# Optimization experiments

Hardware: AMD Instinct MI355X
Metric: run time of the kernel (lower is better)

## Reference

```python
import jax, jax.numpy as jnp
import numpy as np

N, E, C, ED = 50000, 800000, 128, 16
NEG_SLOPE = 0.2


def setup_inputs() -> dict:
    key = jax.random.key(0)
    ks = jax.random.split(key, 18)
    inp = {
        "h": jax.random.normal(ks[0], (N, C), jnp.float32),
        "edge_index": jax.random.randint(ks[1], (2, E), 0, N),
        "edge_attr": jax.random.normal(ks[2], (E, ED), jnp.float32),
        "reducible": jax.random.randint(ks[3], (N,), 0, 2) > 0,
    }
    names = ["W", "att_src", "att_dst", "W_edge", "att_edge", "W_res", "bias"]
    shapes = [(C, C), (C,), (C,), (ED, C), (C,), (C, C), (C,)]
    i = 4
    for pre in ["red_", "irr_"]:
        for n, sh in zip(names, shapes):
            inp[pre + n] = jax.random.normal(ks[i], sh, jnp.float32) * 0.05
            i += 1
    return inp


def _gat_conv(h, src, dst, edge_attr, W, att_src, att_dst, W_edge, att_edge, W_res, bias):
    """PyG GATConv (heads=1, residual=True, add_self_loops=True, fill_value='mean')."""
    n = h.shape[0]
    # self-loop edge_attr = mean of incoming edge_attr per node (0 if none)
    sum_attr = jax.ops.segment_sum(edge_attr, dst, num_segments=n)
    cnt = jax.ops.segment_sum(jnp.ones((edge_attr.shape[0],), edge_attr.dtype), dst, num_segments=n)
    mean_attr = sum_attr / jnp.maximum(cnt, 1.0)[:, None]
    loop = jnp.arange(n)
    s = jnp.concatenate([src, loop])   # [E+N]
    d = jnp.concatenate([dst, loop])   # [E+N]
    ea = jnp.concatenate([edge_attr, mean_attr], axis=0)  # [E+N, ED]
    x = h @ W                              # [N, C]
    a_src = x @ att_src                    # [N]
    a_dst = x @ att_dst                    # [N]
    a_edge = (ea @ W_edge) @ att_edge      # [E+N]
    alpha = jax.nn.leaky_relu(a_src[s] + a_dst[d] + a_edge, NEG_SLOPE)
    # per-destination softmax (every node has a self-loop -> denom > 0)
    m = jax.ops.segment_max(alpha, d, num_segments=n)
    ex = jnp.exp(alpha - m[d])
    denom = jax.ops.segment_sum(ex, d, num_segments=n)
    w = ex / denom[d]                      # [E+N]
    out = jax.ops.segment_sum(w[:, None] * x[s], d, num_segments=n)  # [N, C]
    return out + h @ W_res + bias


def reference(h, edge_index, edge_attr, reducible,
              red_W, red_att_src, red_att_dst, red_W_edge, red_att_edge, red_W_res, red_bias,
              irr_W, irr_att_src, irr_att_dst, irr_W_edge, irr_att_edge, irr_W_res, irr_bias):
    src, dst = edge_index[0], edge_index[1]
    out_r = _gat_conv(h, src, dst, edge_attr, red_W, red_att_src, red_att_dst,
                      red_W_edge, red_att_edge, red_W_res, red_bias)
    out_i = _gat_conv(h, src, dst, edge_attr, irr_W, irr_att_src, irr_att_dst,
                      irr_W_edge, irr_att_edge, irr_W_res, irr_bias)
    return jax.nn.relu(jnp.where(reducible[:, None], out_r, out_i))
```

## Files before the change

kernel.cpp:

```cpp
#include <hip/hip_runtime.h>
#include <hip/hip_bf16.h>

#define CDIM 128
#define EDIM 16
#define NEG_SLOPE 0.2f

typedef __attribute__((ext_vector_type(8))) short bf16x8;
typedef __attribute__((ext_vector_type(4))) float f32x4;
typedef __attribute__((ext_vector_type(2))) float f32x2;
typedef unsigned int uint;
typedef unsigned short ushort;

__device__ __forceinline__ ushort f2bf(float f) {
    uint u = __float_as_uint(f);
    return (ushort)((u + 0x7fffu + ((u >> 16) & 1u)) >> 16);
}
__device__ __forceinline__ uint packbf(float lo, float hi) {
    return ((uint)f2bf(hi) << 16) | (uint)f2bf(lo);
}
__device__ __forceinline__ float bflo(uint w) { return __uint_as_float(w << 16); }
__device__ __forceinline__ float bfhi(uint w) { return __uint_as_float(w & 0xffff0000u); }

__device__ __forceinline__ bool redtest(const void* red, int i, int notInt, int notFloat) {
    if (!notInt)        return ((const int*)red)[i] != 0;
    else if (!notFloat) return ((const float*)red)[i] != 0.f;
    else                return ((const unsigned char*)red)[i] != 0;
}

__global__ void bcatwe_kernel(const float* __restrict__ Wr, const float* __restrict__ Wi,
                              const float* __restrict__ Wrr, const float* __restrict__ Wri,
                              ushort* __restrict__ BT,
                              const float* __restrict__ WeR, const float* __restrict__ aeR,
                              const float* __restrict__ WeI, const float* __restrict__ aeI,
                              float* __restrict__ we) {
    if (blockIdx.x < 256) {
        int idx = blockIdx.x * 256 + threadIdx.x;
        int c = idx >> 7, k = idx & 127;
        const float* srcm;
        if (c < 128)      srcm = Wr;
        else if (c < 256) srcm = Wi;
        else if (c < 384) srcm = Wrr;
        else              srcm = Wri;
        BT[idx] = f2bf(srcm[k * 128 + (c & 127)]);
    } else {
        int lane = threadIdx.x;
        if (lane < 16) {
            float s = 0.f;
            for (int c = 0; c < CDIM; ++c) s += WeR[lane * CDIM + c] * aeR[c];
            we[lane] = s;
        } else if (lane < 32) {
            int j = lane - 16;
            float s = 0.f;
            for (int c = 0; c < CDIM; ++c) s += WeI[j * CDIM + c] * aeI[c];
            we[16 + j] = s;
        }
    }
}

__global__ __launch_bounds__(256) void prep_kernel(const uint* __restrict__ red, int nwords,
                                                   int* __restrict__ flags,
                                                   const int* __restrict__ dst, int* __restrict__ cnt8,
                                                   int* __restrict__ rank,
                                                   const float* __restrict__ ea, const float* __restrict__ we,
                                                   uint* __restrict__ escal4,
                                                   const float* __restrict__ h, ushort* __restrict__ hbf,
                                                   int N, int E, int n4) {
    int i = blockIdx.x * 256 + threadIdx.x;
    int c = blockIdx.x & 7;
    if (i < nwords) {
        uint w = red[i];
        bool isInt = (w <= 1u);
        bool isFloat = (w == 0u) || (w == 0x3f800000u);
        if (!isInt) atomicOr(&flags[0], 1);
        if (!isFloat) atomicOr(&flags[1], 1);
    }
    if (i < E) {
        int d = dst[i];
        int rk = atomicAdd(&cnt8[c * N + d], 1);
        __builtin_nontemporal_store(rk | (c << 28), rank + i);
        const f32x4* row = (const f32x4*)(ea + (size_t)i * EDIM);
        const float4* we4 = (const float4*)we;
        float er = 0.f, ei = 0.f;
#pragma unroll
        for (int q = 0; q < 4; ++q) {
            f32x4 v = __builtin_nontemporal_load(row + q);
            float4 wr = we4[q], wi = we4[4 + q];
            er += v.x * wr.x + v.y * wr.y + v.z * wr.z + v.w * wr.w;
            ei += v.x * wi.x + v.y * wi.y + v.z * wi.z + v.w * wi.w;
        }
        __builtin_nontemporal_store(packbf(er, ei), escal4 + i);
    }
    if (i < n4) {
        f32x4 v = __builtin_nontemporal_load((const f32x4*)h + i);
        uint2 o;
        o.x = packbf(v.x, v.y);
        o.y = packbf(v.z, v.w);
        ((uint2*)hbf)[i] = o;
    }
}

__global__ __launch_bounds__(256) void gemm_dots(const ushort* __restrict__ A,
                                                 const ushort* __restrict__ BT,
                                                 ushort* __restrict__ C,
                                                 const float* __restrict__ attsr, const float* __restrict__ attdr,
                                                 const float* __restrict__ attsi, const float* __restrict__ attdi,
                                                 float* __restrict__ asr, float* __restrict__ adr,
                                                 float* __restrict__ asi, float* __restrict__ adi,
                                                 int M) {
    __shared__ ushort As[128 * 128];
    __shared__ ushort Bs[128 * 128];
    __shared__ float dots[4][128];
    int t = threadIdx.x;
    int lane = t & 63, wv = t >> 6;
    int rb = blockIdx.x * 128;

    if (t < 128) { dots[0][t] = 0.f; dots[1][t] = 0.f; dots[2][t] = 0.f; dots[3][t] = 0.f; }

    int rsub = wv * 4 + (lane >> 4);
    int c0 = lane & 15;
#pragma unroll
    for (int p = 0; p < 8; ++p) {
        int row = p * 16 + rsub;
        int chunk = c0 ^ (row & 7);
        int gra = rb + row; if (gra > M - 1) gra = M - 1;
        const ushort* ga = A + (size_t)gra * 128 + chunk * 8;
        __builtin_amdgcn_global_load_lds(
            (const __attribute__((address_space(1))) void*)ga,
            (__attribute__((address_space(3))) void*)((char*)As + p * 4096 + wv * 1024),
            16, 0, 0);
    }

    int wr = wv >> 1, wc = wv & 1;
    int l15 = lane & 15, l4 = lane >> 4;
    const char* Ab = (const char*)As;
    const char* Bb = (const char*)Bs;

    for (int s = 0; s < 4; ++s) {
#pragma unroll
        for (int p = 0; p < 8; ++p) {
            int row = p * 16 + rsub;
            int chunk = c0 ^ (row & 7);
            const ushort* gb = BT + (size_t)(s * 128 + row) * 128 + chunk * 8;
            __builtin_amdgcn_global_load_lds(
                (const __attribute__((address_space(1))) void*)gb,
                (__attribute__((address_space(3))) void*)((char*)Bs + p * 4096 + wv * 1024),
                16, 0, 0);
        }
        __syncthreads();

        f32x4 acc[4][4];
#pragma unroll
        for (int i = 0; i < 4; ++i)
#pragma unroll
            for (int j = 0; j < 4; ++j) acc[i][j] = (f32x4){0.f, 0.f, 0.f, 0.f};

#pragma unroll
        for (int ks = 0; ks < 4; ++ks) {
            bf16x8 a[4], b[4];
#pragma unroll
            for (int f = 0; f < 4; ++f) {
                int row = wr * 64 + f * 16 + l15;
                int ch = (ks * 4 + l4) ^ (row & 7);
                a[f] = *(const bf16x8*)(Ab + row * 256 + ch * 16);
                int col = wc * 64 + f * 16 + l15;
                int ch2 = (ks * 4 + l4) ^ (col & 7);
                b[f] = *(const bf16x8*)(Bb + col * 256 + ch2 * 16);
            }
#pragma unroll
            for (int i = 0; i < 4; ++i)
#pragma unroll
                for (int j = 0; j < 4; ++j)
                    acc[i][j] = __builtin_amdgcn_mfma_f32_16x16x32_bf16(a[i], b[j], acc[i][j], 0, 0, 0);
        }

        if (s < 2) {
            const float* attS = s ? attsi : attsr;
            const float* attD = s ? attdi : attdr;
            float aS[4], aD[4];
#pragma unroll
            for (int j = 0; j < 4; ++j) {
                int c = wc * 64 + j * 16 + l15;
                aS[j] = attS[c]; aD[j] = attD[c];
            }
#pragma unroll
            for (int i = 0; i < 4; ++i)
#pragma unroll
                for (int rr = 0; rr < 4; ++rr) {
                    float ps = 0.f, pd = 0.f;
#pragma unroll
                    for (int j = 0; j < 4; ++j) {
                        float v = acc[i][j][rr];
                        ps += v * aS[j]; pd += v * aD[j];
                    }
#pragma unroll
                    for (int d = 1; d < 16; d <<= 1) {
                        ps += __shfl_xor(ps, d); pd += __shfl_xor(pd, d);
                    }
                    if (l15 == 0) {
                        int row = wr * 64 + i * 16 + l4 * 4 + rr;
                        atomicAdd(&dots[s * 2 + 0][row], ps);
                        atomicAdd(&dots[s * 2 + 1][row], pd);
                    }
                }
        }

#pragma unroll
        for (int i = 0; i < 4; ++i) {
            int rl = wr * 64 + i * 16 + l4 * 4;
#pragma unroll
            for (int j = 0; j < 4; ++j) {
                int col = s * 128 + wc * 64 + j * 16 + l15;
#pragma unroll
                for (int r = 0; r < 4; ++r) {
                    int gr = rb + rl + r;
                    if (gr < M) C[(size_t)gr * 512 + col] = f2bf(acc[i][j][r]);
                }
            }
        }
        __syncthreads();
    }

    if (t < 128) {
        int gr = rb + t;
        if (gr < M) {
            asr[gr] = dots[0][t]; adr[gr] = dots[1][t];
            asi[gr] = dots[2][t]; adi[gr] = dots[3][t];
        }
    }
}

__global__ __launch_bounds__(256) void scanA_kernel(int* __restrict__ cnt8,
                                                    int* __restrict__ offA,
                                                    int* __restrict__ bsum, int n) {
    __shared__ int wsum[4];
    int t = threadIdx.x, lane = t & 63, wid = t >> 6;
    int i0 = blockIdx.x * 1024 + t * 4;
    int v[4];
#pragma unroll
    for (int j = 0; j < 4; ++j) {
        int d = i0 + j;
        int tot = 0;
        if (d < n) {
#pragma unroll
            for (int x = 0; x < 8; ++x) {
                int cv = cnt8[x * n + d];
                cnt8[x * n + d] = tot;
                tot += cv;
            }
        }
        v[j] = tot;
    }
    int s = v[0] + v[1] + v[2] + v[3];
    int incl = s;
#pragma unroll
    for (int d = 1; d < 64; d <<= 1) { int u = __shfl_up(incl, d); if (lane >= d) incl += u; }
    if (lane == 63) wsum[wid] = incl;
    __syncthreads();
    int wpre = 0;
    for (int w = 0; w < wid; ++w) wpre += wsum[w];
    int run = wpre + incl - s;
#pragma unroll
    for (int j = 0; j < 4; ++j) {
        int i = i0 + j;
        if (i < n) offA[i] = run;
        run += v[j];
    }
    if (t == 255) bsum[blockIdx.x] = wpre + incl;
}

__global__ void scanB_kernel(int* __restrict__ bsum, int nb) {
    int lane = threadIdx.x;
    int carry = 0;
    for (int base = 0; base < nb; base += 64) {
        int i = base + lane;
        int v = (i < nb) ? bsum[i] : 0;
        int incl = v;
#pragma unroll
        for (int d = 1; d < 64; d <<= 1) { int u = __shfl_up(incl, d); if (lane >= d) incl += u; }
        if (i < nb) bsum[i] = carry + incl - v;
        carry += __shfl(incl, 63);
    }
}

__global__ __launch_bounds__(256) void scatter_kernel(
    const int* __restrict__ src, const int* __restrict__ dst,
    const int* __restrict__ rank, const uint* __restrict__ escal4,
    const void* __restrict__ red, const int* __restrict__ flags,
    const int* __restrict__ offA, const int* __restrict__ bsum,
    const int* __restrict__ cnt8,
    uint* __restrict__ csr, int N, int E) {
    int e = blockIdx.x * 256 + threadIdx.x;
    if (e >= E) return;
    int s = __builtin_nontemporal_load(src + e);
    int d = __builtin_nontemporal_load(dst + e);
    uint ee = __builtin_nontemporal_load(escal4 + e);
    int rkw = __builtin_nontemporal_load(rank + e);
    int c = ((uint)rkw) >> 28;
    int rk = rkw & 0x0fffffff;
    int notInt = flags[0], notFloat = flags[1];
    bool rr = redtest(red, d, notInt, notFloat);
    uint evb = rr ? (ee & 0xffffu) : (ee >> 16);
    int off = offA[d] + bsum[d >> 10] + cnt8[c * N + d];
    csr[off + rk] = (uint)s | (evb << 16);
}

__global__ __launch_bounds__(256) void node_kernel(
    const ushort* __restrict__ xcat,
    const float* __restrict__ adst_r, const float* __restrict__ adst_i,
    const float* __restrict__ asrc_r, const float* __restrict__ asrc_i,
    const void* __restrict__ red, const int* __restrict__ flags,
    const int* __restrict__ offA, const int* __restrict__ bsum,
    const uint* __restrict__ csr,
    const float* __restrict__ bias_r, const float* __restrict__ bias_i,
    float* __restrict__ out, int n, int E) {
    __shared__ uint2 buf[4][64];
    int wv = threadIdx.x >> 6, lane = threadIdx.x & 63;
    int node = blockIdx.x * 4 + wv;
    if (node >= n) return;

    int notInt = flags[0], notFloat = flags[1];
    bool r = redtest(red, node, notInt, notFloat);

    const float* asrc = r ? asrc_r : asrc_i;
    float adst = (r ? adst_r : adst_i)[node];
    uint vsel = r ? 0u : 256u;
    int b0 = offA[node] + bsum[node >> 10];
    int b1 = (node + 1 < n) ? (offA[node + 1] + bsum[(node + 1) >> 10]) : E;
    int k = b1 - b0;
    const char* xb = (const char*)xcat;
    uint lane4 = lane * 4;

    float denom_l = 0.f, sumE = 0.f;
    float2 acca = make_float2(0.f, 0.f), accb = make_float2(0.f, 0.f);

    for (int base = b0; base < b1; base += 64) {
        int j = base + lane;
        float ex = 0.f; uint soff = 0;
        if (j < b1) {
            uint rec = __builtin_nontemporal_load(csr + j);
            uint s = rec & 0xffffu;
            float ev = bfhi(rec);
            sumE += ev;
            soff = s * 1024u + vsel;
            float a = asrc[s] + ev + adst;
            float al = (a >= 0.f) ? a : NEG_SLOPE * a;
            ex = __expf(fminf(al, 60.f));
            denom_l += ex;
        }
        buf[wv][lane] = make_uint2(__float_as_uint(ex), soff);
        __builtin_amdgcn_wave_barrier();
        int cc = min(64, b1 - base);
        int ccp = (cc + 7) & ~7;
        for (int tq = 0; tq < ccp; tq += 8) {
            uint2 u[8];
#pragma unroll
            for (int q = 0; q < 8; ++q) u[q] = buf[wv][tq + q];
            uint v[8];
#pragma unroll
            for (int q = 0; q < 8; ++q) v[q] = *(const uint*)(xb + u[q].y + lane4);
#pragma unroll
            for (int q = 0; q < 4; ++q) {
                float w = __uint_as_float(u[q].x);
                acca.x += w * bflo(v[q]); acca.y += w * bfhi(v[q]);
            }
#pragma unroll
            for (int q = 4; q < 8; ++q) {
                float w = __uint_as_float(u[q].x);
                accb.x += w * bflo(v[q]); accb.y += w * bfhi(v[q]);
            }
        }
        __builtin_amdgcn_wave_barrier();
    }
    float acc0 = acca.x + accb.x, acc1 = acca.y + accb.y;

#pragma unroll
    for (int d = 32; d; d >>= 1) {
        sumE += __shfl_xor(sumE, d);
        denom_l += __shfl_xor(denom_l, d);
    }

    float eself = sumE / fmaxf((float)k, 1.f);
    float a = asrc[node] + adst + eself;
    float aself = (a >= 0.f) ? a : NEG_SLOPE * a;
    float exl = __expf(fminf(aself, 60.f));
    float denom = denom_l + exl;
    uint voff = (uint)node * 1024u + vsel;
    uint vsw = *(const uint*)(xb + voff + lane4);
    acc0 += exl * bflo(vsw);
    acc1 += exl * bfhi(vsw);

    float inv = 1.f / denom;
    uint roff = (uint)node * 1024u + (r ? 512u : 768u);
    uint bw = *(const uint*)(xb + roff + lane4);
    float2 bi2 = ((const float2*)(r ? bias_r : bias_i))[lane];
    f32x2 o;
    o.x = fmaxf(acc0 * inv + bflo(bw) + bi2.x, 0.f);
    o.y = fmaxf(acc1 * inv + bfhi(bw) + bi2.y, 0.f);
    __builtin_nontemporal_store(o, ((f32x2*)out) + (size_t)node * 64 + lane);
}

extern "C" void kernel_launch(void* const* d_in, const int* in_sizes, int n_in,
                              void* d_out, int out_size, void* d_ws, size_t ws_size,
                              hipStream_t stream) {
    const float* h          = (const float*)d_in[0];
    const int*   edge_index = (const int*)d_in[1];
    const float* edge_attr  = (const float*)d_in[2];
    const void*  reducible  = d_in[3];
    const float* red_W      = (const float*)d_in[4];
    const float* red_att_src= (const float*)d_in[5];
    const float* red_att_dst= (const float*)d_in[6];
    const float* red_W_edge = (const float*)d_in[7];
    const float* red_att_edge=(const float*)d_in[8];
    const float* red_W_res  = (const float*)d_in[9];
    const float* red_bias   = (const float*)d_in[10];
    const float* irr_W      = (const float*)d_in[11];
    const float* irr_att_src= (const float*)d_in[12];
    const float* irr_att_dst= (const float*)d_in[13];
    const float* irr_W_edge = (const float*)d_in[14];
    const float* irr_att_edge=(const float*)d_in[15];
    const float* irr_W_res  = (const float*)d_in[16];
    const float* irr_bias   = (const float*)d_in[17];

    const int N = in_sizes[0] / CDIM;
    const int E = in_sizes[1] / 2;
    const int* src = edge_index;
    const int* dst = edge_index + E;
    const int nb = (N + 1023) / 1024;
    const int n4 = N * 128 / 4;

    float* out = (float*)d_out;

    size_t cur = 0;
    auto alloc = [&](size_t bytes) { size_t p = cur; cur = (cur + bytes + 255) & ~(size_t)255; return p; };
    char* ws = (char*)d_ws;
    size_t o_xcat  = alloc((size_t)N * 512 * 2);
    size_t o_hbf   = alloc((size_t)N * 128 * 2);
    size_t o_bcat  = alloc(512 * 128 * 2);
    size_t o_we    = alloc(256);
    size_t o_asr   = alloc((size_t)N * 4);
    size_t o_adr   = alloc((size_t)N * 4);
    size_t o_asi   = alloc((size_t)N * 4);
    size_t o_adi   = alloc((size_t)N * 4);
    size_t o_flags = alloc(256);
    size_t o_cnt8  = alloc((size_t)N * 8 * 4);
    size_t o_offA  = alloc((size_t)N * 4);
    size_t o_bsum  = alloc((size_t)(nb + 1) * 4);
    size_t o_rank  = alloc((size_t)E * 4);
    size_t o_escal = alloc((size_t)E * 4);
    size_t o_csr   = alloc((size_t)E * 4);
    if (cur > ws_size) return;

    ushort* xcat = (ushort*)(ws + o_xcat);
    ushort* hbf  = (ushort*)(ws + o_hbf);
    ushort* bcat = (ushort*)(ws + o_bcat);
    float* we    = (float*)(ws + o_we);
    float* asr   = (float*)(ws + o_asr);
    float* adr   = (float*)(ws + o_adr);
    float* asi   = (float*)(ws + o_asi);
    float* adi   = (float*)(ws + o_adi);
    int*   flags = (int*)(ws + o_flags);
    int*   cnt8  = (int*)(ws + o_cnt8);
    int*   offA  = (int*)(ws + o_offA);
    int*   bsum  = (int*)(ws + o_bsum);
    int*   rank  = (int*)(ws + o_rank);
    uint*  escal4= (uint*)(ws + o_escal);
    uint*  csr   = (uint*)(ws + o_csr);

    hipMemsetAsync(flags, 0, 8, stream);
    hipMemsetAsync(cnt8, 0, (size_t)N * 8 * 4, stream);

    bcatwe_kernel<<<257, 256, 0, stream>>>(red_W, irr_W, red_W_res, irr_W_res, bcat,
                                           red_W_edge, red_att_edge, irr_W_edge, irr_att_edge, we);

    int nwords = N / 4;
    int pgrid = (max(E, n4) + 255) / 256;
    prep_kernel<<<pgrid, 256, 0, stream>>>((const uint*)reducible, nwords, flags,
                                           dst, cnt8, rank, edge_attr, we, escal4,
                                           h, hbf, N, E, n4);

    gemm_dots<<<(N + 127) / 128, 256, 0, stream>>>(hbf, bcat, xcat,
                                                   red_att_src, red_att_dst,
                                                   irr_att_src, irr_att_dst,
                                                   asr, adr, asi, adi, N);

    scanA_kernel<<<nb, 256, 0, stream>>>(cnt8, offA, bsum, N);
    scanB_kernel<<<1, 64, 0, stream>>>(bsum, nb);

    scatter_kernel<<<(E + 255) / 256, 256, 0, stream>>>(src, dst, rank, escal4,
                                                        reducible, flags, offA, bsum, cnt8,
                                                        csr, N, E);

    node_kernel<<<(N + 3) / 4, 256, 0, stream>>>(xcat, adr, adi, asr, asi,
                                                 reducible, flags, offA, bsum, csr,
                                                 red_bias, irr_bias, out, N, E);
}
```

Before: 152.4 us.

## Fuse prep, scan and CSR scatter into one cooperative grid-synced kernel

Replaces the separate prep, two scan and scatter kernels with a single cooperative kernel that uses grid.sync between phases. Each thread keeps its edges' src, dst, rank and edge scalar in registers, so the rank and escal intermediate arrays are no longer written and re-read. The memsets are folded into the weight-prep kernel. In exchange it adds three grid-wide barriers and a fixed grid of 1024 blocks with 4 edges per thread. The second-level scan assumes nb is at most 64.

Measured after the change: 492.6 us. +223.2%, slower.

```diff
diff --git a/kernel.cpp b/kernel.cpp
--- a/kernel.cpp
+++ b/kernel.cpp
@@ -1,9 +1,12 @@
 #include <hip/hip_runtime.h>
 #include <hip/hip_bf16.h>
+#include <hip/hip_cooperative_groups.h>
 
 #define CDIM 128
 #define EDIM 16
 #define NEG_SLOPE 0.2f
+
+namespace cg = cooperative_groups;
 
 typedef __attribute__((ext_vector_type(8))) short bf16x8;
 typedef __attribute__((ext_vector_type(4))) float f32x4;
@@ -32,7 +35,11 @@
                               ushort* __restrict__ BT,
                               const float* __restrict__ WeR, const float* __restrict__ aeR,
                               const float* __restrict__ WeI, const float* __restrict__ aeI,
-                              float* __restrict__ we) {
+                              float* __restrict__ we,
+                              int* __restrict__ cnt8, int* __restrict__ flags, int N8) {
+    int gtid = blockIdx.x * 256 + threadIdx.x;
+    for (int i = gtid; i < N8; i += gridDim.x * 256) cnt8[i] = 0;
+    if (gtid == 0) { flags[0] = 0; flags[1] = 0; }
     if (blockIdx.x < 256) {
         int idx = blockIdx.x * 256 + threadIdx.x;
         int c = idx >> 7, k = idx & 127;
@@ -42,7 +49,7 @@
         else if (c < 384) srcm = Wrr;
         else              srcm = Wri;
         BT[idx] = f2bf(srcm[k * 128 + (c & 127)]);
-    } else {
+    } else if (blockIdx.x == 256) {
         int lane = threadIdx.x;
         if (lane < 16) {
             float s = 0.f;
@@ -57,45 +64,122 @@
     }
 }
 
-__global__ __launch_bounds__(256) void prep_kernel(const uint* __restrict__ red, int nwords,
-                                                   int* __restrict__ flags,
-                                                   const int* __restrict__ dst, int* __restrict__ cnt8,
-                                                   int* __restrict__ rank,
-                                                   const float* __restrict__ ea, const float* __restrict__ we,
-                                                   uint* __restrict__ escal4,
-                                                   const float* __restrict__ h, ushort* __restrict__ hbf,
-                                                   int N, int E, int n4) {
-    int i = blockIdx.x * 256 + threadIdx.x;
+#define FB 1024
+#define EPT 4
+__global__ __launch_bounds__(256, 4) void fused_kernel(
+    const uint* __restrict__ red, int nwords, int* __restrict__ flags,
+    const int* __restrict__ src, const int* __restrict__ dst, int* __restrict__ cnt8,
+    const float* __restrict__ ea, const float* __restrict__ we,
+    const float* __restrict__ h, ushort* __restrict__ hbf,
+    int* __restrict__ offA, int* __restrict__ bsum,
+    uint* __restrict__ csr, int N, int E, int n4, int nb) {
+    cg::grid_group grid = cg::this_grid();
+    int tid = blockIdx.x * 256 + threadIdx.x;
     int c = blockIdx.x & 7;
-    if (i < nwords) {
-        uint w = red[i];
+    const int STRIDE = FB * 256;
+
+    if (tid < nwords) {
+        uint w = red[tid];
         bool isInt = (w <= 1u);
         bool isFloat = (w == 0u) || (w == 0x3f800000u);
         if (!isInt) atomicOr(&flags[0], 1);
         if (!isFloat) atomicOr(&flags[1], 1);
     }
-    if (i < E) {
-        int d = dst[i];
-        int rk = atomicAdd(&cnt8[c * N + d], 1);
-        __builtin_nontemporal_store(rk | (c << 28), rank + i);
-        const f32x4* row = (const f32x4*)(ea + (size_t)i * EDIM);
-        const float4* we4 = (const float4*)we;
-        float er = 0.f, ei = 0.f;
-#pragma unroll
-        for (int q = 0; q < 4; ++q) {
-            f32x4 v = __builtin_nontemporal_load(row + q);
-            float4 wr = we4[q], wi = we4[4 + q];
-            er += v.x * wr.x + v.y * wr.y + v.z * wr.z + v.w * wr.w;
-            ei += v.x * wi.x + v.y * wi.y + v.z * wi.z + v.w * wi.w;
-        }
-        __builtin_nontemporal_store(packbf(er, ei), escal4 + i);
-    }
-    if (i < n4) {
+
+    int sA[EPT], dA[EPT], rkA[EPT];
+    uint eeA[EPT];
+    const float4* we4 = (const float4*)we;
+#pragma unroll
+    for (int k = 0; k < EPT; ++k) {
+        int e = tid + k * STRIDE;
+        dA[k] = -1;
+        if (e < E) {
+            int d = dst[e];
+            sA[k] = src[e];
+            dA[k] = d;
+            rkA[k] = atomicAdd(&cnt8[c * N + d], 1);
+            const f32x4* row = (const f32x4*)(ea + (size_t)e * EDIM);
+            float er = 0.f, ei = 0.f;
+#pragma unroll
+            for (int q = 0; q < 4; ++q) {
+                f32x4 v = __builtin_nontemporal_load(row + q);
+                float4 wr = we4[q], wi = we4[4 + q];
+                er += v.x * wr.x + v.y * wr.y + v.z * wr.z + v.w * wr.w;
+                ei += v.x * wi.x + v.y * wi.y + v.z * wi.z + v.w * wi.w;
+            }
+            eeA[k] = packbf(er, ei);
+        }
+    }
+    for (int i = tid; i < n4; i += STRIDE) {
         f32x4 v = __builtin_nontemporal_load((const f32x4*)h + i);
         uint2 o;
         o.x = packbf(v.x, v.y);
         o.y = packbf(v.z, v.w);
         ((uint2*)hbf)[i] = o;
+    }
+
+    grid.sync();
+
+    if (blockIdx.x < nb) {
+        __shared__ int wsum[4];
+        int t = threadIdx.x, lane = t & 63, wid = t >> 6;
+        int i0 = blockIdx.x * 1024 + t * 4;
+        int v[4];
+#pragma unroll
+        for (int j = 0; j < 4; ++j) {
+            int d = i0 + j;
+            int tot = 0;
+            if (d < N) {
+#pragma unroll
+                for (int x = 0; x < 8; ++x) {
+                    int cv = cnt8[x * N + d];
+                    cnt8[x * N + d] = tot;
+                    tot += cv;
+                }
+            }
+            v[j] = tot;
+        }
+        int s = v[0] + v[1] + v[2] + v[3];
+        int incl = s;
+#pragma unroll
+        for (int d = 1; d < 64; d <<= 1) { int u = __shfl_up(incl, d); if (lane >= d) incl += u; }
+        if (lane == 63) wsum[wid] = incl;
+        __syncthreads();
+        int wpre = 0;
+        for (int w = 0; w < wid; ++w) wpre += wsum[w];
+        int run = wpre + incl - s;
+#pragma unroll
+        for (int j = 0; j < 4; ++j) {
+            int i = i0 + j;
+            if (i < N) offA[i] = run;
+            run += v[j];
+        }
+        if (t == 255) bsum[blockIdx.x] = wpre + incl;
+    }
+
+    grid.sync();
+
+    if (blockIdx.x == 0 && threadIdx.x < 64) {
+        int lane = threadIdx.x;
+        int v = (lane < nb) ? bsum[lane] : 0;
+        int incl = v;
+#pragma unroll
+        for (int d = 1; d < 64; d <<= 1) { int u = __shfl_up(incl, d); if (lane >= d) incl += u; }
+        if (lane < nb) bsum[lane] = incl - v;
+    }
+
+    grid.sync();
+
+    int notInt = flags[0], notFloat = flags[1];
+#pragma unroll
+    for (int k = 0; k < EPT; ++k) {
+        if (dA[k] >= 0) {
+            int d = dA[k];
+            bool rr = redtest(red, d, notInt, notFloat);
+            uint evb = rr ? (eeA[k] & 0xffffu) : (eeA[k] >> 16);
+            int off = offA[d] + bsum[d >> 10] + cnt8[c * N + d] + rkA[k];
+            csr[off] = (uint)sA[k] | (evb << 16);
+        }
     }
 }
 
@@ -227,81 +311,6 @@
             asi[gr] = dots[2][t]; adi[gr] = dots[3][t];
         }
     }
-}
-
-__global__ __launch_bounds__(256) void scanA_kernel(int* __restrict__ cnt8,
-                                                    int* __restrict__ offA,
-                                                    int* __restrict__ bsum, int n) {
-    __shared__ int wsum[4];
-    int t = threadIdx.x, lane = t & 63, wid = t >> 6;
-    int i0 = blockIdx.x * 1024 + t * 4;
-    int v[4];
-#pragma unroll
-    for (int j = 0; j < 4; ++j) {
-        int d = i0 + j;
-        int tot = 0;
-        if (d < n) {
-#pragma unroll
-            for (int x = 0; x < 8; ++x) {
-                int cv = cnt8[x * n + d];
-                cnt8[x * n + d] = tot;
-                tot += cv;
-            }
-        }
-        v[j] = tot;
-    }
-    int s = v[0] + v[1] + v[2] + v[3];
-    int incl = s;
-#pragma unroll
-    for (int d = 1; d < 64; d <<= 1) { int u = __shfl_up(incl, d); if (lane >= d) incl += u; }
-    if (lane == 63) wsum[wid] = incl;
-    __syncthreads();
-    int wpre = 0;
-    for (int w = 0; w < wid; ++w) wpre += wsum[w];
-    int run = wpre + incl - s;
-#pragma unroll
-    for (int j = 0; j < 4; ++j) {
-        int i = i0 + j;
-        if (i < n) offA[i] = run;
-        run += v[j];
-    }
-    if (t == 255) bsum[blockIdx.x] = wpre + incl;
-}
-
-__global__ void scanB_kernel(int* __restrict__ bsum, int nb) {
-    int lane = threadIdx.x;
-    int carry = 0;
-    for (int base = 0; base < nb; base += 64) {
-        int i = base + lane;
-        int v = (i < nb) ? bsum[i] : 0;
-        int incl = v;
-#pragma unroll
-        for (int d = 1; d < 64; d <<= 1) { int u = __shfl_up(incl, d); if (lane >= d) incl += u; }
-        if (i < nb) bsum[i] = carry + incl - v;
-        carry += __shfl(incl, 63);
-    }
-}
-
-__global__ __launch_bounds__(256) void scatter_kernel(
-    const int* __restrict__ src, const int* __restrict__ dst,
-    const int* __restrict__ rank, const uint* __restrict__ escal4,
-    const void* __restrict__ red, const int* __restrict__ flags,
-    const int* __restrict__ offA, const int* __restrict__ bsum,
-    const int* __restrict__ cnt8,
-    uint* __restrict__ csr, int N, int E) {
-    int e = blockIdx.x * 256 + threadIdx.x;
-    if (e >= E) return;
-    int s = __builtin_nontemporal_load(src + e);
-    int d = __builtin_nontemporal_load(dst + e);
-    uint ee = __builtin_nontemporal_load(escal4 + e);
-    int rkw = __builtin_nontemporal_load(rank + e);
-    int c = ((uint)rkw) >> 28;
-    int rk = rkw & 0x0fffffff;
-    int notInt = flags[0], notFloat = flags[1];
-    bool rr = redtest(red, d, notInt, notFloat);
-    uint evb = rr ? (ee & 0xffffu) : (ee >> 16);
-    int off = offA[d] + bsum[d >> 10] + cnt8[c * N + d];
-    csr[off + rk] = (uint)s | (evb << 16);
 }
 
 __global__ __launch_bounds__(256) void node_kernel(
@@ -445,8 +454,6 @@
     size_t o_cnt8  = alloc((size_t)N * 8 * 4);
     size_t o_offA  = alloc((size_t)N * 4);
     size_t o_bsum  = alloc((size_t)(nb + 1) * 4);
-    size_t o_rank  = alloc((size_t)E * 4);
-    size_t o_escal = alloc((size_t)E * 4);
     size_t o_csr   = alloc((size_t)E * 4);
     if (cur > ws_size) return;
 
@@ -462,34 +469,42 @@
     int*   cnt8  = (int*)(ws + o_cnt8);
     int*   offA  = (int*)(ws + o_offA);
     int*   bsum  = (int*)(ws + o_bsum);
-    int*   rank  = (int*)(ws + o_rank);
-    uint*  escal4= (uint*)(ws + o_escal);
     uint*  csr   = (uint*)(ws + o_csr);
 
-    hipMemsetAsync(flags, 0, 8, stream);
-    hipMemsetAsync(cnt8, 0, (size_t)N * 8 * 4, stream);
-
+    int N8 = N * 8;
     bcatwe_kernel<<<257, 256, 0, stream>>>(red_W, irr_W, red_W_res, irr_W_res, bcat,
-                                           red_W_edge, red_att_edge, irr_W_edge, irr_att_edge, we);
+                                           red_W_edge, red_att_edge, irr_W_edge, irr_att_edge, we,
+                                           cnt8, flags, N8);
 
     int nwords = N / 4;
-    int pgrid = (max(E, n4) + 255) / 256;
-    prep_kernel<<<pgrid, 256, 0, stream>>>((const uint*)reducible, nwords, flags,
-                                           dst, cnt8, rank, edge_attr, we, escal4,
-                                           h, hbf, N, E, n4);
+    {
+        const uint* redw = (const uint*)reducible;
+        int* flagsp = flags;
+        const int* srcp = src;
+        const int* dstp = dst;
+        int* cnt8p = cnt8;
+        const float* eap = edge_attr;
+        const float* wep = we;
+        const float* hp = h;
+        ushort* hbfp = hbf;
+        int* offAp = offA;
+        int* bsump = bsum;
+        uint* csrp = csr;
+        int Nv = N, Ev = E, n4v = n4, nbv = nb, nwordsv = nwords;
+        void* args[] = { (void*)&redw, (void*)&nwordsv, (void*)&flagsp,
+                         (void*)&srcp, (void*)&dstp, (void*)&cnt8p,
+                         (void*)&eap, (void*)&wep,
+                         (void*)&hp, (void*)&hbfp,
+                         (void*)&offAp, (void*)&bsump,
+                         (void*)&csrp, (void*)&Nv, (void*)&Ev, (void*)&n4v, (void*)&nbv };
+        hipLaunchCooperativeKernel((void*)fused_kernel, dim3(FB), dim3(256), args, 0, stream);
+    }
 
     gemm_dots<<<(N + 127) / 128, 256, 0, stream>>>(hbf, bcat, xcat,
                                                    red_att_src, red_att_dst,
                                                    irr_att_src, irr_att_dst,
                                                    asr, adr, asi, adi, N);
 
-    scanA_kernel<<<nb, 256, 0, stream>>>(cnt8, offA, bsum, N);
-    scanB_kernel<<<1, 64, 0, stream>>>(bsum, nb);
-
-    scatter_kernel<<<(E + 255) / 256, 256, 0, stream>>>(src, dst, rank, escal4,
-                                                        reducible, flags, offA, bsum, cnt8,
-                                                        csr, N, E);
-
     node_kernel<<<(N + 3) / 4, 256, 0, stream>>>(xcat, adr, adi, asr, asi,
                                                  reducible, flags, offA, bsum, csr,
                                                  red_bias, irr_bias, out, N, E);
```
